# Performance work log

Measured on AMD Instinct MI355X. Metric: run time of the kernel, lower is better.

The kernel has to match this reference:

```python
import jax, jax.numpy as jnp
import numpy as np

B, S, D = 2, 2048, 2048
H = 16
Q_LORA, KV_LORA = 1536, 512
D_NOPE, D_ROPE = 128, 64
D_QK = D_NOPE + D_ROPE  # 192
D_V = 128
EPS = 1e-6
SCALE = D_QK ** -0.5


def rms_norm(x, w):
    var = jnp.mean(jnp.square(x), axis=-1, keepdims=True)
    return x * jax.lax.rsqrt(var + EPS) * w


def apply_rotary_emb(x, freqs_cis):
    # x: [B, S, h, dr]; freqs_cis: [S, dr//2, 2] (cos, sin); interleaved pairs
    b, s, h, dr = x.shape
    xp = x.reshape(b, s, h, dr // 2, 2)
    x0, x1 = xp[..., 0], xp[..., 1]
    cos = freqs_cis[None, :, None, :, 0]
    sin = freqs_cis[None, :, None, :, 1]
    o0 = x0 * cos - x1 * sin
    o1 = x0 * sin + x1 * cos
    return jnp.stack([o0, o1], axis=-1).reshape(b, s, h, dr)


def setup_inputs() -> dict:
    key = jax.random.key(0)
    ks = jax.random.split(key, 8)
    std = 0.02
    x = jax.random.normal(ks[0], (B, S, D), jnp.float32)
    inv_freq = 1.0 / (10000.0 ** (np.arange(0, D_ROPE, 2, dtype=np.float32) / D_ROPE))
    ang = np.outer(np.arange(S, dtype=np.float32), inv_freq)  # [S, 32]
    freqs_cis = jnp.asarray(np.stack([np.cos(ang), np.sin(ang)], axis=-1))
    return {
        'x': x,
        'freqs_cis': freqs_cis,
        'Wqa': jax.random.normal(ks[1], (Q_LORA, D), jnp.float32) * std,
        'q_a_ln_w': jnp.ones((Q_LORA,), jnp.float32),
        'Wqb': jax.random.normal(ks[2], (H * D_QK, Q_LORA), jnp.float32) * std,
        'Wkva': jax.random.normal(ks[3], (KV_LORA + D_ROPE, D), jnp.float32) * std,
        'kv_a_ln_w': jnp.ones((KV_LORA,), jnp.float32),
        'Wkvb': jax.random.normal(ks[4], (H * (D_NOPE + D_V), KV_LORA), jnp.float32) * std,
        'Wo': jax.random.normal(ks[5], (D, H * D_V), jnp.float32) * std,
    }


def reference(x, freqs_cis, Wqa, q_a_ln_w, Wqb, Wkva, kv_a_ln_w, Wkvb, Wo):
    # Low-rank Q projection: down -> RMSNorm -> up
    q = rms_norm(jnp.einsum('bsd,rd->bsr', x, Wqa), q_a_ln_w)
    q = jnp.einsum('bsr,er->bse', q, Wqb).reshape(B, S, H, D_QK)
    q_nope, q_pe = q[..., :D_NOPE], q[..., D_NOPE:]
    q = jnp.concatenate([q_nope, apply_rotary_emb(q_pe, freqs_cis)], axis=-1)

    # Low-rank KV projection with shared (MQA) rope part
    kv = jnp.einsum('bsd,ed->bse', x, Wkva)
    kv_c, k_pe = kv[..., :KV_LORA], kv[..., KV_LORA:]
    kv_c = rms_norm(kv_c, kv_a_ln_w)
    k_pe = apply_rotary_emb(k_pe[:, :, None, :], freqs_cis)  # [B,S,1,D_ROPE]
    kv = jnp.einsum('bsr,er->bse', kv_c, Wkvb).reshape(B, S, H, D_NOPE + D_V)
    k_nope, v = kv[..., :D_NOPE], kv[..., D_NOPE:]
    k = jnp.concatenate(
        [k_nope, jnp.broadcast_to(k_pe, (B, S, H, D_ROPE))], axis=-1)

    # Causal SDPA with scale = qk_head_dim ** -0.5
    scores = jnp.einsum('bqhd,bkhd->bhqk', q, k) * SCALE
    causal = jnp.tril(jnp.ones((S, S), bool))
    scores = jnp.where(causal[None, None], scores, jnp.finfo(scores.dtype).min)
    probs = jax.nn.softmax(scores, axis=-1)
    out = jnp.einsum('bhqk,bkhd->bqhd', probs, v).reshape(B, S, H * D_V)
    return jnp.einsum('bse,de->bsd', out, Wo)
```

## Files before the change

### kernel.cpp

```cpp
#include <hip/hip_runtime.h>
#include <math.h>

#define B_ 2
#define S_ 2048
#define D_ 2048
#define H_ 16
#define QLORA 1536
#define KVLORA 512
#define DN 128
#define DR 64
#define DQK 192
#define DV 128
#define EPSF 1e-6f
#define SCALEF 0.07216878364870322f

typedef short short8 __attribute__((ext_vector_type(8)));
typedef float float4v __attribute__((ext_vector_type(4)));

__device__ __forceinline__ unsigned short f2bf(float f) {
    union { float f; unsigned u; } x; x.f = f;
    unsigned r = x.u + 0x7fffu + ((x.u >> 16) & 1u);
    return (unsigned short)(r >> 16);
}
__device__ __forceinline__ float bf2f(unsigned short u) {
    union { unsigned u; float f; } x; x.u = (unsigned)u << 16;
    return x.f;
}

#define GLD16(src, dst)                                                        \
    __builtin_amdgcn_global_load_lds(                                          \
        (const __attribute__((address_space(1))) void*)(src),                  \
        (__attribute__((address_space(3))) void*)(dst), 16, 0, 0)

__global__ __launch_bounds__(256) void conv_all(
        const float* __restrict__ s0, unsigned short* __restrict__ d0, long e0,
        const float* __restrict__ s1, unsigned short* __restrict__ d1, long e1,
        const float* __restrict__ s2, unsigned short* __restrict__ d2, long e2,
        const float* __restrict__ s3, unsigned short* __restrict__ d3, long e3,
        const float* __restrict__ s4, unsigned short* __restrict__ d4, long e4,
        const float* __restrict__ s5, unsigned short* __restrict__ d5) {
    long c = (long)blockIdx.x * 256 + threadIdx.x;
    const float* src;
    unsigned short* dst;
    if      (c < e0) { src = s0; dst = d0; }
    else if (c < e1) { src = s1; dst = d1; c -= e0; }
    else if (c < e2) { src = s2; dst = d2; c -= e1; }
    else if (c < e3) { src = s3; dst = d3; c -= e2; }
    else if (c < e4) { src = s4; dst = d4; c -= e3; }
    else             { src = s5; dst = d5; c -= e4; }
    const float* p = src + c * 8;
    float4 a = *(const float4*)(p);
    float4 b = *(const float4*)(p + 4);
    union { short8 v; unsigned short u[8]; } t;
    t.u[0] = f2bf(a.x); t.u[1] = f2bf(a.y); t.u[2] = f2bf(a.z); t.u[3] = f2bf(a.w);
    t.u[4] = f2bf(b.x); t.u[5] = f2bf(b.y); t.u[6] = f2bf(b.z); t.u[7] = f2bf(b.w);
    *(short8*)&dst[c * 8] = t.v;
}

#define GBM 128
#define GBN 128
#define GBK 64

template <typename OT>
__global__ __launch_bounds__(256) void gemm_t(const unsigned short* __restrict__ A,
                                              const unsigned short* __restrict__ W,
                                              OT* __restrict__ C,
                                              int M, int N, int K) {
    __shared__ unsigned short As[GBM * GBK];
    __shared__ unsigned short Ws[GBN * GBK];

    const int tid = threadIdx.x;
    const int w = tid >> 6, lane = tid & 63;
    const int l16 = lane & 15, quad = lane >> 4;
    const int wm = (w >> 1) * 64, wn = (w & 1) * 64;
    const int row0 = blockIdx.y * GBM, col0 = blockIdx.x * GBN;

    const int rL  = lane >> 3;
    const int c8g = (lane & 7) ^ rL;
    const int swzk[2] = { (((0 * 4) + quad) ^ (l16 & 7)) * 8,
                          (((1 * 4) + quad) ^ (l16 & 7)) * 8 };

    const float4v zf = {0.f, 0.f, 0.f, 0.f};
    float4v acc[4][4] = {{zf, zf, zf, zf}, {zf, zf, zf, zf},
                         {zf, zf, zf, zf}, {zf, zf, zf, zf}};

    for (int k0 = 0; k0 < K; k0 += GBK) {
        __syncthreads();
#pragma unroll
        for (int j = 0; j < 4; ++j) {
            const int ch = w * 4 + j;
            const int r = ch * 8 + rL;
            GLD16(&A[(size_t)(row0 + r) * K + k0 + c8g * 8], &As[ch * 512]);
            GLD16(&W[(size_t)(col0 + r) * K + k0 + c8g * 8], &Ws[ch * 512]);
        }
        __syncthreads();

#pragma unroll
        for (int kk = 0; kk < 2; ++kk) {
            const int swz = swzk[kk];
            short8 af[4], bf[4];
#pragma unroll
            for (int mi = 0; mi < 4; ++mi)
                af[mi] = *(const short8*)&As[(wm + mi * 16 + l16) * GBK + swz];
#pragma unroll
            for (int ni = 0; ni < 4; ++ni)
                bf[ni] = *(const short8*)&Ws[(wn + ni * 16 + l16) * GBK + swz];
#pragma unroll
            for (int mi = 0; mi < 4; ++mi)
#pragma unroll
                for (int ni = 0; ni < 4; ++ni)
                    acc[mi][ni] = __builtin_amdgcn_mfma_f32_16x16x32_bf16(af[mi], bf[ni], acc[mi][ni], 0, 0, 0);
        }
    }

#pragma unroll
    for (int mi = 0; mi < 4; ++mi)
#pragma unroll
        for (int ni = 0; ni < 4; ++ni)
#pragma unroll
            for (int r = 0; r < 4; ++r) {
                size_t idx = (size_t)(row0 + wm + mi * 16 + quad * 4 + r) * N + col0 + wn + ni * 16 + l16;
                if constexpr (sizeof(OT) == 2) C[idx] = f2bf(acc[mi][ni][r]);
                else                           C[idx] = acc[mi][ni][r];
            }
}

#define TBM 256
#define TBN 256
#define TBK 64

template <int MODE>
__global__ __launch_bounds__(512, 2) void gemm8(const unsigned short* __restrict__ A,
                                                const unsigned short* __restrict__ W,
                                                void* __restrict__ Cp,
                                                unsigned short* __restrict__ Cs,
                                                int M, int N, int K) {
    __shared__ unsigned short As[2][TBM * TBK];
    __shared__ unsigned short Ws[2][TBN * TBK];

    const int tid = threadIdx.x;
    const int w = tid >> 6, lane = tid & 63;
    const int l16 = lane & 15, quad = lane >> 4;
    const int wm = (w >> 2) * 128, wn = (w & 3) * 64;
    const int row0 = blockIdx.y * TBM, col0 = blockIdx.x * TBN;
    const int NT = K / TBK;

    auto stage = [&](int t_, int bufi) {
        const int k0 = t_ * TBK;
#pragma unroll
        for (int i_ = 0; i_ < 4; ++i_) {
            const int ch = i_ * 512 + w * 64 + lane;
            const int r_ = ch >> 3, c_ = ch & 7;
            GLD16(&A[(size_t)(row0 + r_) * K + k0 + ((c_ ^ (r_ & 7)) << 3)],
                  &As[bufi][(i_ * 512 + w * 64) * 8]);
        }
#pragma unroll
        for (int i_ = 0; i_ < 4; ++i_) {
            const int ch = i_ * 512 + w * 64 + lane;
            const int r_ = ch >> 3, c_ = ch & 7;
            GLD16(&W[(size_t)(col0 + r_) * K + k0 + ((c_ ^ (r_ & 7)) << 3)],
                  &Ws[bufi][(i_ * 512 + w * 64) * 8]);
        }
    };

    const float4v zf = {0.f, 0.f, 0.f, 0.f};
    float4v acc[8][4];
#pragma unroll
    for (int mi = 0; mi < 8; ++mi)
#pragma unroll
        for (int ni = 0; ni < 4; ++ni) acc[mi][ni] = zf;

    stage(0, 0);
    stage(1, 1);
    asm volatile("s_waitcnt vmcnt(8)" ::: "memory");
    __builtin_amdgcn_sched_barrier(0);
    __builtin_amdgcn_s_barrier();
    __builtin_amdgcn_sched_barrier(0);

    for (int t = 0; t < NT; ++t) {
        const int buf = t & 1;
        const unsigned short* Ab = As[buf];
        const unsigned short* Wb = Ws[buf];

        short8 bfr[2][4];
#pragma unroll
        for (int kk = 0; kk < 2; ++kk)
#pragma unroll
            for (int ni = 0; ni < 4; ++ni) {
                const int Rn = wn + ni * 16 + l16;
                bfr[kk][ni] = *(const short8*)&Wb[Rn * TBK + (((kk * 4 + quad) ^ (l16 & 7)) << 3)];
            }
#pragma unroll
        for (int mi = 0; mi < 8; ++mi) {
            const int Rm = wm + mi * 16 + l16;
            short8 a0 = *(const short8*)&Ab[Rm * TBK + (((0 + quad) ^ (l16 & 7)) << 3)];
            short8 a1 = *(const short8*)&Ab[Rm * TBK + (((4 + quad) ^ (l16 & 7)) << 3)];
#pragma unroll
            for (int ni = 0; ni < 4; ++ni) {
                acc[mi][ni] = __builtin_amdgcn_mfma_f32_16x16x32_bf16(a0, bfr[0][ni], acc[mi][ni], 0, 0, 0);
                acc[mi][ni] = __builtin_amdgcn_mfma_f32_16x16x32_bf16(a1, bfr[1][ni], acc[mi][ni], 0, 0, 0);
            }
        }

        __builtin_amdgcn_s_barrier();
        if (t + 2 < NT) {
            stage(t + 2, buf);
            asm volatile("s_waitcnt vmcnt(8)" ::: "memory");
        } else if (t + 1 < NT) {
            asm volatile("s_waitcnt vmcnt(0)" ::: "memory");
        }
        __builtin_amdgcn_sched_barrier(0);
        __builtin_amdgcn_s_barrier();
        __builtin_amdgcn_sched_barrier(0);
    }

#pragma unroll
    for (int mi = 0; mi < 8; ++mi)
#pragma unroll
        for (int ni = 0; ni < 4; ++ni)
#pragma unroll
            for (int r = 0; r < 4; ++r) {
                const int row = row0 + wm + mi * 16 + quad * 4 + r;
                const int col = col0 + wn + ni * 16 + l16;
                if constexpr (MODE == 0) {
                    ((float*)Cp)[(size_t)row * N + col] = acc[mi][ni][r];
                } else if constexpr (MODE == 1) {
                    ((unsigned short*)Cp)[(size_t)row * N + col] = f2bf(acc[mi][ni][r]);
                } else {
                    const int h = col >> 8, within = col & 255;
                    const unsigned short v = f2bf(acc[mi][ni][r]);
                    if (within < 128) {
                        const int b = row >> 11, s = row & (S_ - 1);
                        Cs[((size_t)(b * H_ + h) * S_ + s) * DQK + within] = v;
                    } else {
                        ((unsigned short*)Cp)[(size_t)row * N + col] = v;
                    }
                }
            }
}

__global__ __launch_bounds__(256) void rmsnorm_b(const float* __restrict__ X,
                                                 const float* __restrict__ w,
                                                 unsigned short* __restrict__ Y,
                                                 int n, int ld) {
    __shared__ float tmp[4];
    const int row = blockIdx.x;
    const int tid = threadIdx.x;
    const float* x = X + (size_t)row * ld;

    float ss = 0.f;
    for (int c = tid; c < n; c += 256) {
        float v = x[c];
        ss = fmaf(v, v, ss);
    }
#pragma unroll
    for (int off = 32; off; off >>= 1) ss += __shfl_xor(ss, off, 64);
    if ((tid & 63) == 0) tmp[tid >> 6] = ss;
    __syncthreads();
    ss = tmp[0] + tmp[1] + tmp[2] + tmp[3];
    float r = rsqrtf(ss / (float)n + EPSF);

    for (int c = tid; c < n; c += 256)
        Y[(size_t)row * n + c] = f2bf(x[c] * r * w[c]);
}

__global__ __launch_bounds__(256) void kv_post(const float* __restrict__ KV,
                                               const float* __restrict__ w,
                                               const float* __restrict__ fc,
                                               unsigned short* __restrict__ kvcb,
                                               unsigned short* __restrict__ Kbf,
                                               int ldkv) {
    __shared__ float tmp[4];
    const int row = blockIdx.x;
    const int s = row & (S_ - 1);
    const int b = row >> 11;
    const int tid = threadIdx.x;
    const float* kv = KV + (size_t)row * ldkv;

    float ss = 0.f;
#pragma unroll
    for (int c = tid; c < KVLORA; c += 256) {
        float v = kv[c];
        ss = fmaf(v, v, ss);
    }
#pragma unroll
    for (int off = 32; off; off >>= 1) ss += __shfl_xor(ss, off, 64);
    if ((tid & 63) == 0) tmp[tid >> 6] = ss;
    __syncthreads();
    ss = tmp[0] + tmp[1] + tmp[2] + tmp[3];
    float r = rsqrtf(ss / (float)KVLORA + EPSF);

#pragma unroll
    for (int c = tid; c < KVLORA; c += 256)
        kvcb[(size_t)row * KVLORA + c] = f2bf(kv[c] * r * w[c]);

    if (tid < 32) {
        int i = tid;
        float c0 = fc[(s * 32 + i) * 2 + 0];
        float s0 = fc[(s * 32 + i) * 2 + 1];
        float x0 = kv[KVLORA + 2 * i];
        float x1 = kv[KVLORA + 2 * i + 1];
        unsigned short b0 = f2bf(x0 * c0 - x1 * s0);
        unsigned short b1 = f2bf(x0 * s0 + x1 * c0);
#pragma unroll
        for (int h = 0; h < H_; ++h) {
            unsigned short* kp = Kbf + ((size_t)(b * H_ + h) * S_ + s) * DQK + DN;
            kp[2 * i]     = b0;
            kp[2 * i + 1] = b1;
        }
    }
}

__global__ __launch_bounds__(256) void pack_vt(const unsigned short* __restrict__ kvbb,
                                               unsigned short* __restrict__ Vt) {
    __shared__ unsigned short T[DV][72];
    const int st = blockIdx.x;
    const int bh = blockIdx.y;
    const int b = bh >> 4, h = bh & 15;
    const int s0 = st * 64;
    const int tid = threadIdx.x;

    for (int c = tid; c < 64 * 16; c += 256) {
        int sp = c >> 4, ch = c & 15;
        short8 v = *(const short8*)&kvbb[(size_t)(b * S_ + s0 + sp) * (H_ * 256) + h * 256 + DN + ch * 8];
        union { short8 v; unsigned short u[8]; } t; t.v = v;
        int dv = ch * 8;
#pragma unroll
        for (int e = 0; e < 8; ++e) T[dv + e][sp] = t.u[e];
    }
    __syncthreads();
    for (int c = tid; c < 128 * 8; c += 256) {
        int dv = c >> 3, ch = c & 7;
        *(short8*)&Vt[((size_t)bh * DV + dv) * S_ + s0 + ch * 8] = *(short8*)&T[dv][ch * 8];
    }
}

#define QTILES 16
#define PROW 76

__global__ __launch_bounds__(512, 1) void flash_mfma(const unsigned short* __restrict__ Qb,
                                                     const float* __restrict__ fc,
                                                     const unsigned short* __restrict__ Kbf,
                                                     const unsigned short* __restrict__ Vt,
                                                     unsigned short* __restrict__ Ob) {
    __shared__ unsigned short Ks[2][64 * 192];
    __shared__ unsigned short Vs[2][128 * 64];
    __shared__ unsigned short Ps[8][16][PROW];

    const int bh = blockIdx.x;
    const int bx = blockIdx.y;
    const int b = bh >> 4, h = bh & 15;
    const int tid = threadIdx.x;
    const int w = tid >> 6, lane = tid & 63;
    const int l16 = lane & 15, quad = lane >> 4;
    const int sw = l16 & 7;

    const unsigned short* Kg = Kbf + (size_t)bh * S_ * DQK;
    const unsigned short* Vg = Vt + (size_t)bh * DV * S_;

    auto stage = [&](int kt_, int bufi) {
        const int kb_ = kt_ * 64;
#pragma unroll
        for (int i_ = 0; i_ < 3; ++i_) {
            int ch = (w * 3 + i_) * 64 + lane;
            int r_ = ch / 24, c_ = ch - r_ * 24;
            GLD16(&Kg[(size_t)(kb_ + r_) * DQK + ((c_ ^ (r_ & 7)) << 3)],
                  &Ks[bufi][(w * 3 + i_) * 512]);
        }
#pragma unroll
        for (int i_ = 0; i_ < 2; ++i_) {
            int ch = (w * 2 + i_) * 64 + lane;
            int r_ = ch >> 3, c_ = ch & 7;
            GLD16(&Vg[(size_t)r_ * S_ + kb_ + ((c_ ^ (r_ & 7)) << 3)],
                  &Vs[bufi][(w * 2 + i_) * 512]);
        }
    };

    for (int half = 0; half < 2; ++half) {
        const int qt = half ? (QTILES - 1 - bx) : bx;
        const int q0 = qt * 128;
        const int ntiles = 2 * qt + 2;
        const int wr0 = q0 + w * 16;

        stage(0, 0);

        short8 a_q[6];
        {
            const int s = wr0 + l16;
            const unsigned short* qrow = Qb + (size_t)(b * S_ + s) * (H_ * DQK) + h * DQK;
#pragma unroll
            for (int i = 0; i < 6; ++i) {
                short8 t = *(const short8*)&qrow[i * 32 + quad * 8];
                if (i >= 4) {
                    union { short8 v; unsigned short u[8]; } x; x.v = t;
#pragma unroll
                    for (int j = 0; j < 4; ++j) {
                        int ip = (i - 4) * 16 + quad * 4 + j;
                        float c0 = fc[(s * 32 + ip) * 2 + 0];
                        float s0 = fc[(s * 32 + ip) * 2 + 1];
                        float x0 = bf2f(x.u[2 * j]);
                        float x1 = bf2f(x.u[2 * j + 1]);
                        x.u[2 * j]     = f2bf(x0 * c0 - x1 * s0);
                        x.u[2 * j + 1] = f2bf(x0 * s0 + x1 * c0);
                    }
                    t = x.v;
                }
                a_q[i] = t;
            }
        }

        const float4v zf = {0.f, 0.f, 0.f, 0.f};
        float4v o_acc[8] = {zf, zf, zf, zf, zf, zf, zf, zf};
        float l_r[4] = {0.f, 0.f, 0.f, 0.f};

        int buf = 0;
        for (int kt = 0; kt < ntiles; ++kt) {
            const int kb = kt * 64;

            __builtin_amdgcn_s_barrier();
            if (kt + 1 < ntiles) {
                stage(kt + 1, buf ^ 1);
                asm volatile("s_waitcnt vmcnt(5)" ::: "memory");
            } else {
                asm volatile("s_waitcnt vmcnt(0)" ::: "memory");
            }
            __builtin_amdgcn_sched_barrier(0);
            __builtin_amdgcn_s_barrier();
            __builtin_amdgcn_sched_barrier(0);

            if (kb <= wr0 + 15) {
                const unsigned short* Kb_ = Ks[buf];
                const unsigned short* Vb_ = Vs[buf];

                float4v sc[4] = {zf, zf, zf, zf};
#pragma unroll
                for (int i = 0; i < 6; ++i) {
                    short8 bk[4];
#pragma unroll
                    for (int kg = 0; kg < 4; ++kg)
                        bk[kg] = *(const short8*)&Kb_[(kg * 16 + l16) * 192 + (((i * 4 + quad) ^ sw) << 3)];
#pragma unroll
                    for (int kg = 0; kg < 4; ++kg)
                        sc[kg] = __builtin_amdgcn_mfma_f32_16x16x32_bf16(a_q[i], bk[kg], sc[kg], 0, 0, 0);
                }

                const bool mneed = (kb + 63 > wr0);
#pragma unroll
                for (int kg = 0; kg < 4; ++kg) {
                    const int key = kb + kg * 16 + l16;
#pragma unroll
                    for (int r = 0; r < 4; ++r) {
                        float p = __expf(sc[kg][r] * SCALEF);
                        if (mneed && key > wr0 + quad * 4 + r) p = 0.f;
                        l_r[r] += p;
                        Ps[w][quad * 4 + r][kg * 16 + l16] = f2bf(p);
                    }
                }

#pragma unroll
                for (int kc = 0; kc < 2; ++kc) {
                    short8 pa = *(const short8*)&Ps[w][l16][kc * 32 + quad * 8];
#pragma unroll
                    for (int dvt = 0; dvt < 8; ++dvt) {
                        short8 vb = *(const short8*)&Vb_[(dvt * 16 + l16) * 64 + (((kc * 4 + quad) ^ sw) << 3)];
                        o_acc[dvt] = __builtin_amdgcn_mfma_f32_16x16x32_bf16(pa, vb, o_acc[dvt], 0, 0, 0);
                    }
                }
            }
            buf ^= 1;
        }

#pragma unroll
        for (int r = 0; r < 4; ++r) {
            float t = l_r[r];
            t += __shfl_xor(t, 1);
            t += __shfl_xor(t, 2);
            t += __shfl_xor(t, 4);
            t += __shfl_xor(t, 8);
            l_r[r] = t;
        }
#pragma unroll
        for (int r = 0; r < 4; ++r) {
            float inv = 1.f / l_r[r];
            int row = wr0 + quad * 4 + r;
            unsigned short* op = Ob + (size_t)(b * S_ + row) * (H_ * DV) + h * DV;
#pragma unroll
            for (int dvt = 0; dvt < 8; ++dvt)
                op[dvt * 16 + l16] = f2bf(o_acc[dvt][r] * inv);
        }
    }
}

extern "C" void kernel_launch(void* const* d_in, const int* in_sizes, int n_in,
                              void* d_out, int out_size, void* d_ws, size_t ws_size,
                              hipStream_t stream) {
    const float* x    = (const float*)d_in[0];
    const float* fc   = (const float*)d_in[1];
    const float* Wqa  = (const float*)d_in[2];
    const float* qlw  = (const float*)d_in[3];
    const float* Wqb  = (const float*)d_in[4];
    const float* Wkva = (const float*)d_in[5];
    const float* kvw  = (const float*)d_in[6];
    const float* Wkvb = (const float*)d_in[7];
    const float* Wo   = (const float*)d_in[8];
    float* out = (float*)d_out;

    const int M = B_ * S_;
    const int NQKV = QLORA + 640;
    char* wsb = (char*)d_ws;

    unsigned short* qb  = (unsigned short*)wsb;
    unsigned short* Wob = (unsigned short*)(wsb + 25165824);
    char* R2 = wsb + 50331648;
    float*          qlkv  = (float*)R2;
    unsigned short* xb    = (unsigned short*)(R2 + 35651584);
    unsigned short* Wcat  = (unsigned short*)(R2 + 52428800);
    unsigned short* kvbb  = (unsigned short*)R2;
    unsigned short* attnb = (unsigned short*)R2;
    char* R3 = R2 + 67108864;
    unsigned short* qlatb = (unsigned short*)R3;
    unsigned short* Wqbb  = (unsigned short*)(R3 + 12582912);
    unsigned short* Kbf   = (unsigned short*)R3;
    char* R4 = R3 + 25165824;
    unsigned short* kvcb  = (unsigned short*)(R4 + 1048576);
    unsigned short* Wkvbb = (unsigned short*)(R4 + 5242880);
    unsigned short* Vt    = (unsigned short*)R4;

    {
        const long e0 = 1048576;
        const long e1 = e0 + 393216;
        const long e2 = e1 + 147456;
        const long e3 = e2 + 589824;
        const long e4 = e3 + 262144;
        const long tot = e4 + 524288;
        conv_all<<<(int)(tot / 256), 256, 0, stream>>>(
            x, xb, e0,
            Wqa, Wcat, e1,
            Wkva, Wcat + (size_t)QLORA * D_, e2,
            Wqb, Wqbb, e3,
            Wkvb, Wkvbb, e4,
            Wo, Wob);
    }

    gemm_t<float><<<dim3(NQKV / GBN, M / GBM), 256, 0, stream>>>(xb, Wcat, qlkv, M, NQKV, D_);

    rmsnorm_b<<<M, 256, 0, stream>>>(qlkv, qlw, qlatb, QLORA, NQKV);

    gemm8<1><<<dim3(H_ * DQK / TBN, M / TBM), 512, 0, stream>>>(qlatb, Wqbb, qb, nullptr, M, H_ * DQK, QLORA);

    kv_post<<<M, 256, 0, stream>>>(qlkv + QLORA, kvw, fc, kvcb, Kbf, NQKV);

    gemm8<2><<<dim3(H_ * 256 / TBN, M / TBM), 512, 0, stream>>>(kvcb, Wkvbb, kvbb, Kbf, M, H_ * 256, KVLORA);

    pack_vt<<<dim3(S_ / 64, B_ * H_), 256, 0, stream>>>(kvbb, Vt);

    flash_mfma<<<dim3(B_ * H_, QTILES / 2), 512, 0, stream>>>(qb, fc, Kbf, Vt, attnb);

    gemm8<0><<<dim3(D_ / TBN, M / TBM), 512, 0, stream>>>(attnb, Wob, out, nullptr, M, D_, D_);
}
```

Baseline: 447.4 us.

## Triple-buffer flash K/V staging and narrow output GEMM tile to 128 columns

The flash attention kernel moves from double to triple buffering of K/V tiles in shared memory. Each tile is now prefetched two iterations ahead, and only one barrier per iteration sits after compute rather than before it, so loads overlap more with MFMA work. The gemm8 kernel is templated on its N tile width, and the output projection uses a 256x128 tile, which doubles its block count to fill more CUs. The costs are more LDS use in flash (which may limit occupancy) and more reloading of A in the output GEMM.

```diff
diff --git a/kernel.cpp b/kernel.cpp
--- a/kernel.cpp
+++ b/kernel.cpp
@@ -126,23 +126,25 @@
 }
 
 #define TBM 256
-#define TBN 256
 #define TBK 64
 
-template <int MODE>
+template <int MODE, int BN>
 __global__ __launch_bounds__(512, 2) void gemm8(const unsigned short* __restrict__ A,
                                                 const unsigned short* __restrict__ W,
                                                 void* __restrict__ Cp,
                                                 unsigned short* __restrict__ Cs,
                                                 int M, int N, int K) {
+    constexpr int NWCH = BN / 64;
+    constexpr int MF = (BN == 256) ? 8 : 4;
     __shared__ unsigned short As[2][TBM * TBK];
-    __shared__ unsigned short Ws[2][TBN * TBK];
+    __shared__ unsigned short Ws[2][BN * TBK];
 
     const int tid = threadIdx.x;
     const int w = tid >> 6, lane = tid & 63;
     const int l16 = lane & 15, quad = lane >> 4;
-    const int wm = (w >> 2) * 128, wn = (w & 3) * 64;
-    const int row0 = blockIdx.y * TBM, col0 = blockIdx.x * TBN;
+    const int wm = (BN == 256) ? (w >> 2) * 128 : (w >> 1) * 64;
+    const int wn = (BN == 256) ? (w & 3) * 64 : (w & 1) * 64;
+    const int row0 = blockIdx.y * TBM, col0 = blockIdx.x * BN;
     const int NT = K / TBK;
 
     auto stage = [&](int t_, int bufi) {
@@ -155,7 +157,7 @@
                   &As[bufi][(i_ * 512 + w * 64) * 8]);
         }
 #pragma unroll
-        for (int i_ = 0; i_ < 4; ++i_) {
+        for (int i_ = 0; i_ < NWCH; ++i_) {
             const int ch = i_ * 512 + w * 64 + lane;
             const int r_ = ch >> 3, c_ = ch & 7;
             GLD16(&W[(size_t)(col0 + r_) * K + k0 + ((c_ ^ (r_ & 7)) << 3)],
@@ -164,15 +166,16 @@
     };
 
     const float4v zf = {0.f, 0.f, 0.f, 0.f};
-    float4v acc[8][4];
-#pragma unroll
-    for (int mi = 0; mi < 8; ++mi)
+    float4v acc[MF][4];
+#pragma unroll
+    for (int mi = 0; mi < MF; ++mi)
 #pragma unroll
         for (int ni = 0; ni < 4; ++ni) acc[mi][ni] = zf;
 
     stage(0, 0);
     stage(1, 1);
-    asm volatile("s_waitcnt vmcnt(8)" ::: "memory");
+    if constexpr (BN == 256) asm volatile("s_waitcnt vmcnt(8)" ::: "memory");
+    else                     asm volatile("s_waitcnt vmcnt(6)" ::: "memory");
     __builtin_amdgcn_sched_barrier(0);
     __builtin_amdgcn_s_barrier();
     __builtin_amdgcn_sched_barrier(0);
@@ -191,7 +194,7 @@
                 bfr[kk][ni] = *(const short8*)&Wb[Rn * TBK + (((kk * 4 + quad) ^ (l16 & 7)) << 3)];
             }
 #pragma unroll
-        for (int mi = 0; mi < 8; ++mi) {
+        for (int mi = 0; mi < MF; ++mi) {
             const int Rm = wm + mi * 16 + l16;
             short8 a0 = *(const short8*)&Ab[Rm * TBK + (((0 + quad) ^ (l16 & 7)) << 3)];
             short8 a1 = *(const short8*)&Ab[Rm * TBK + (((4 + quad) ^ (l16 & 7)) << 3)];
@@ -205,7 +208,8 @@
         __builtin_amdgcn_s_barrier();
         if (t + 2 < NT) {
             stage(t + 2, buf);
-            asm volatile("s_waitcnt vmcnt(8)" ::: "memory");
+            if constexpr (BN == 256) asm volatile("s_waitcnt vmcnt(8)" ::: "memory");
+            else                     asm volatile("s_waitcnt vmcnt(6)" ::: "memory");
         } else if (t + 1 < NT) {
             asm volatile("s_waitcnt vmcnt(0)" ::: "memory");
         }
@@ -215,7 +219,7 @@
     }
 
 #pragma unroll
-    for (int mi = 0; mi < 8; ++mi)
+    for (int mi = 0; mi < MF; ++mi)
 #pragma unroll
         for (int ni = 0; ni < 4; ++ni)
 #pragma unroll
@@ -343,8 +347,8 @@
                                                      const unsigned short* __restrict__ Kbf,
                                                      const unsigned short* __restrict__ Vt,
                                                      unsigned short* __restrict__ Ob) {
-    __shared__ unsigned short Ks[2][64 * 192];
-    __shared__ unsigned short Vs[2][128 * 64];
+    __shared__ unsigned short Ks[3][64 * 192];
+    __shared__ unsigned short Vs[3][128 * 64];
     __shared__ unsigned short Ps[8][16][PROW];
 
     const int bh = blockIdx.x;
@@ -381,8 +385,6 @@
         const int q0 = qt * 128;
         const int ntiles = 2 * qt + 2;
         const int wr0 = q0 + w * 16;
-
-        stage(0, 0);
 
         short8 a_q[6];
         {
@@ -409,28 +411,29 @@
             }
         }
 
+        stage(0, 0);
+        if (ntiles > 1) stage(1, 1);
+        asm volatile("s_waitcnt vmcnt(5)" ::: "memory");
+        __builtin_amdgcn_sched_barrier(0);
+        __builtin_amdgcn_s_barrier();
+        __builtin_amdgcn_sched_barrier(0);
+
         const float4v zf = {0.f, 0.f, 0.f, 0.f};
         float4v o_acc[8] = {zf, zf, zf, zf, zf, zf, zf, zf};
         float l_r[4] = {0.f, 0.f, 0.f, 0.f};
 
-        int buf = 0;
+        int cb = 0;
         for (int kt = 0; kt < ntiles; ++kt) {
             const int kb = kt * 64;
 
-            __builtin_amdgcn_s_barrier();
-            if (kt + 1 < ntiles) {
-                stage(kt + 1, buf ^ 1);
-                asm volatile("s_waitcnt vmcnt(5)" ::: "memory");
-            } else {
-                asm volatile("s_waitcnt vmcnt(0)" ::: "memory");
-            }
-            __builtin_amdgcn_sched_barrier(0);
-            __builtin_amdgcn_s_barrier();
-            __builtin_amdgcn_sched_barrier(0);
+            if (kt + 2 < ntiles) {
+                int sb = cb + 2; if (sb >= 3) sb -= 3;
+                stage(kt + 2, sb);
+            }
 
             if (kb <= wr0 + 15) {
-                const unsigned short* Kb_ = Ks[buf];
-                const unsigned short* Vb_ = Vs[buf];
+                const unsigned short* Kb_ = Ks[cb];
+                const unsigned short* Vb_ = Vs[cb];
 
                 float4v sc[4] = {zf, zf, zf, zf};
 #pragma unroll
@@ -467,7 +470,17 @@
                     }
                 }
             }
-            buf ^= 1;
+
+            if (kt + 2 < ntiles) {
+                asm volatile("s_waitcnt vmcnt(5)" ::: "memory");
+            } else if (kt + 1 < ntiles) {
+                asm volatile("s_waitcnt vmcnt(0)" ::: "memory");
+            }
+            __builtin_amdgcn_sched_barrier(0);
+            __builtin_amdgcn_s_barrier();
+            __builtin_amdgcn_sched_barrier(0);
+
+            cb = (cb == 2) ? 0 : cb + 1;
         }
 
 #pragma unroll
@@ -546,15 +559,15 @@
 
     rmsnorm_b<<<M, 256, 0, stream>>>(qlkv, qlw, qlatb, QLORA, NQKV);
 
-    gemm8<1><<<dim3(H_ * DQK / TBN, M / TBM), 512, 0, stream>>>(qlatb, Wqbb, qb, nullptr, M, H_ * DQK, QLORA);
+    gemm8<1, 256><<<dim3(H_ * DQK / 256, M / TBM), 512, 0, stream>>>(qlatb, Wqbb, qb, nullptr, M, H_ * DQK, QLORA);
 
     kv_post<<<M, 256, 0, stream>>>(qlkv + QLORA, kvw, fc, kvcb, Kbf, NQKV);
 
-    gemm8<2><<<dim3(H_ * 256 / TBN, M / TBM), 512, 0, stream>>>(kvcb, Wkvbb, kvbb, Kbf, M, H_ * 256, KVLORA);
+    gemm8<2, 256><<<dim3(H_ * 256 / 256, M / TBM), 512, 0, stream>>>(kvcb, Wkvbb, kvbb, Kbf, M, H_ * 256, KVLORA);
 
     pack_vt<<<dim3(S_ / 64, B_ * H_), 256, 0, stream>>>(kvbb, Vt);
 
     flash_mfma<<<dim3(B_ * H_, QTILES / 2), 512, 0, stream>>>(qb, fc, Kbf, Vt, attnb);
 
-    gemm8<0><<<dim3(D_ / TBN, M / TBM), 512, 0, stream>>>(attnb, Wob, out, nullptr, M, D_, D_);
-}
+    gemm8<0, 128><<<dim3(D_ / 128, M / TBM), 512, 0, stream>>>(attnb, Wob, out, nullptr, M, D_, D_);
+}
```

After: 436.9 us. -2.4%, faster.
